# Performance work log

Measured on AMD Instinct MI355X. Metric: run time of the kernel, lower is better.

Reference implementation:

```python
import jax, jax.numpy as jnp
import numpy as np

B, N, C, H, P, DP = 2, 1024, 768, 12, 4, 64
CH = C // H
SCALE = CH ** -0.5
EPS = 1e-5


def setup_inputs() -> dict:
    key = jax.random.key(0)
    ks = jax.random.split(key, 24)
    w = lambda k, s: jax.random.normal(k, s, jnp.float32) * 0.02
    inp = {
        'single': jax.random.normal(ks[0], (B, N, C), jnp.float32),
        'pair': jax.random.normal(ks[1], (B, N, N, DP), jnp.float32),
        'rot': jax.random.normal(ks[2], (B, N, 3, 3), jnp.float32),
        'trans': jax.random.normal(ks[3], (B, N, 3), jnp.float32),
        'mask': jnp.ones((B, N), dtype=bool),
        'Wq': w(ks[4], (C, C)), 'bq': jnp.zeros((C,), jnp.float32),
        'Wk': w(ks[5], (C, C)), 'bk': jnp.zeros((C,), jnp.float32),
        'Wv': w(ks[6], (C, C)), 'bv': jnp.zeros((C,), jnp.float32),
        'Wpb': w(ks[7], (DP, H)), 'bpb': jnp.zeros((H,), jnp.float32),
        'Wqp': w(ks[8], (C, H * P * 3)), 'bqp': jnp.zeros((H * P * 3,), jnp.float32),
        'Wkp': w(ks[9], (C, H * P * 3)), 'bkp': jnp.zeros((H * P * 3,), jnp.float32),
        'Wvp': w(ks[10], (C, H * P * 3)), 'bvp': jnp.zeros((H * P * 3,), jnp.float32),
        'Wo': w(ks[11], (C, C)), 'bo': jnp.zeros((C,), jnp.float32),
        'Wpo': w(ks[12], (H * P * 3, C)), 'bpo': jnp.zeros((C,), jnp.float32),
        'gamma': jnp.ones((C,), jnp.float32), 'beta': jnp.zeros((C,), jnp.float32),
    }
    return inp


def _ipa(single, pair, rot, trans, mask,
         Wq, bq, Wk, bk, Wv, bv, Wpb, bpb,
         Wqp, bqp, Wkp, bkp, Wvp, bvp,
         Wo, bo, Wpo, bpo, gamma, beta):
    # scalar q/k/v: [B,N,H,CH]
    q = (single @ Wq + bq).reshape(B, N, H, CH)
    k = (single @ Wk + bk).reshape(B, N, H, CH)
    v = (single @ Wv + bv).reshape(B, N, H, CH)
    # pair bias: [B,H,N,N]
    pair_bias = jnp.transpose(pair @ Wpb + bpb, (0, 3, 1, 2))
    # point q/k/v in local frames: [B,N,H,P,3]
    q_pts = (single @ Wqp + bqp).reshape(B, N, H, P, 3)
    k_pts = (single @ Wkp + bkp).reshape(B, N, H, P, 3)
    v_pts = (single @ Wvp + bvp).reshape(B, N, H, P, 3)
    # rotate into global frame and translate
    t = trans[:, :, None, None, :]  # [B,N,1,1,3]
    rt = lambda pts: jnp.einsum('bnhpd,bnde->bnhpe', pts, rot) + t
    q_pts, k_pts, v_pts = rt(q_pts), rt(k_pts), rt(v_pts)
    # squared norms: [B,H,N]
    q2 = jnp.transpose((q_pts ** 2).sum((3, 4)), (0, 2, 1))
    k2 = jnp.transpose((k_pts ** 2).sum((3, 4)), (0, 2, 1))
    # logits [B,H,M,N]
    scalar_logits = jnp.einsum('bmhc,bnhc->bhmn', q, k) * SCALE
    qk_pts = jnp.einsum('bmhpd,bnhpd->bhmn', q_pts, k_pts)
    point_logits = -0.5 * (q2[:, :, :, None] + k2[:, :, None, :] - 2.0 * qk_pts) * SCALE
    logits = scalar_logits + point_logits + pair_bias
    mask2d = mask[:, None, :, None] & mask[:, None, None, :]
    logits = jnp.where(mask2d, logits, -1e9)
    attn = jax.nn.softmax(logits, axis=-1)
    # dual output aggregation
    out_scalar = jnp.einsum('bhmn,bnhc->bmhc', attn, v).reshape(B, N, C)
    out_points = jnp.einsum('bhmn,bnhpd->bmhpd', attn, v_pts).reshape(B, N, H * P * 3)
    out = (out_scalar @ Wo + bo) + (out_points @ Wpo + bpo)
    x = single + out
    mu = x.mean(-1, keepdims=True)
    var = ((x - mu) ** 2).mean(-1, keepdims=True)
    return (x - mu) * jax.lax.rsqrt(var + EPS) * gamma + beta


def reference(single, pair, rot, trans, mask,
              Wq, bq, Wk, bk, Wv, bv, Wpb, bpb,
              Wqp, bqp, Wkp, bkp, Wvp, bvp,
              Wo, bo, Wpo, bpo, gamma, beta):
    return _ipa(single, pair, rot, trans, mask,
                Wq, bq, Wk, bk, Wv, bv, Wpb, bpb,
                Wqp, bqp, Wkp, bkp, Wvp, bvp,
                Wo, bo, Wpo, bpo, gamma, beta)
```

## Files before the change

kernel.cpp:

```cpp
#include <hip/hip_runtime.h>
#include <hip/hip_bf16.h>

#define B_ 2
#define N_ 1024
#define C_ 768
#define H_ 12
#define CH_ 64
#define P_ 4
#define DP_ 64
#define HP3 144
#define SCALE_ 0.125f
#define FATS 2816
#define K2_ 960

typedef __attribute__((ext_vector_type(8))) short short8;
typedef __attribute__((ext_vector_type(4))) float f32x4;

__device__ __forceinline__ short f2bf(float f) {
  __hip_bfloat16 h = __float2bfloat16(f);
  return *reinterpret_cast<short*>(&h);
}
__device__ __forceinline__ float bf2f(unsigned short u) {
  __hip_bfloat16 h;
  *reinterpret_cast<unsigned short*>(&h) = u;
  return __bfloat162float(h);
}

__global__ __launch_bounds__(256) void convert_single(
    const float* __restrict__ src, unsigned short* __restrict__ dst)
{
  const int idx = blockIdx.x * 256 + threadIdx.x;
  const float4 v = reinterpret_cast<const float4*>(src)[idx];
  union { unsigned short u[4]; uint2 v2; } o;
  o.u[0] = (unsigned short)f2bf(v.x); o.u[1] = (unsigned short)f2bf(v.y);
  o.u[2] = (unsigned short)f2bf(v.z); o.u[3] = (unsigned short)f2bf(v.w);
  reinterpret_cast<uint2*>(dst)[idx] = o.v2;
}

__global__ __launch_bounds__(256) void pack_w1(
    const float* __restrict__ Wq, const float* __restrict__ Wk,
    const float* __restrict__ Wv, const float* __restrict__ Wqp,
    const float* __restrict__ Wkp, const float* __restrict__ Wvp,
    unsigned short* __restrict__ WT)
{
  __shared__ float t[16][17];
  const int tid = threadIdx.x;
  const int rr = tid >> 4, cc = tid & 15;
  const int kk0 = blockIdx.x * 16;
  const int nn0 = blockIdx.y * 16;
  const float* W = nullptr; int ncol0 = 0, Nw = 768;
  if (nn0 < 2304) {
    int s = nn0 / 768;
    W = (s == 0) ? Wq : (s == 1 ? Wk : Wv);
    ncol0 = nn0 - s * 768; Nw = 768;
  } else if (nn0 < 2736) {
    int s = (nn0 - 2304) / 144;
    W = (s == 0) ? Wqp : (s == 1 ? Wkp : Wvp);
    ncol0 = nn0 - 2304 - s * 144; Nw = 144;
  }
  t[rr][cc] = W ? W[(size_t)(kk0 + rr) * Nw + ncol0 + cc] : 0.f;
  __syncthreads();
  WT[(size_t)(nn0 + rr) * 768 + kk0 + cc] = (unsigned short)f2bf(t[cc][rr]);
}

__global__ __launch_bounds__(256) void pack_w2(
    const float* __restrict__ Wo, const float* __restrict__ Wpo,
    unsigned short* __restrict__ WT)
{
  __shared__ float t[16][17];
  const int tid = threadIdx.x;
  const int rr = tid >> 4, cc = tid & 15;
  const int kk0 = blockIdx.x * 16;
  const int nn0 = blockIdx.y * 16;
  const int k2 = kk0 + rr, h = k2 / 80, c80 = k2 - h * 80;
  float v = 0.f;
  if (c80 < 64)      v = Wo[(size_t)(h * 64 + c80) * 768 + nn0 + cc];
  else if (c80 < 76) v = Wpo[(size_t)(h * 12 + c80 - 64) * 768 + nn0 + cc];
  t[rr][cc] = v;
  __syncthreads();
  WT[(size_t)(nn0 + rr) * 960 + kk0 + cc] = (unsigned short)f2bf(t[cc][rr]);
}

__global__ __launch_bounds__(256) void pack_bias(
    const float* __restrict__ bq, const float* __restrict__ bk,
    const float* __restrict__ bv, const float* __restrict__ bqp,
    const float* __restrict__ bkp, const float* __restrict__ bvp,
    const float* __restrict__ bo, const float* __restrict__ bpo,
    float* __restrict__ bcat1, float* __restrict__ bias2)
{
  const int idx = blockIdx.x * 256 + threadIdx.x;
  if (idx < 2816) {
    float v = 0.f;
    if (idx < 2304) { int s = idx / 768; const float* p = s == 0 ? bq : (s == 1 ? bk : bv); v = p[idx - s * 768]; }
    else if (idx < 2736) { int s = (idx - 2304) / 144; const float* p = s == 0 ? bqp : (s == 1 ? bkp : bvp); v = p[idx - 2304 - s * 144]; }
    bcat1[idx] = v;
  }
  if (idx < 768) bias2[idx] = bo[idx] + bpo[idx];
}

__global__ __launch_bounds__(256) void gemm_bf16(
    const unsigned short* __restrict__ A, int lda,
    const unsigned short* __restrict__ BT, int ldb, int K,
    float* __restrict__ out, int ldo, const float* __restrict__ bias)
{
  __shared__ __align__(16) unsigned short As[128][40];
  __shared__ __align__(16) unsigned short Bs[128][40];
  const int tid = threadIdx.x;
  const int w = tid >> 6, l = tid & 63, r16 = l & 15, g = l >> 4;
  const int wr = w >> 1, wc = w & 1;
  const int bm = blockIdx.y * 128, bn = blockIdx.x * 128;
  f32x4 acc[4][4];
  #pragma unroll
  for (int mi = 0; mi < 4; ++mi)
    #pragma unroll
    for (int nj = 0; nj < 4; ++nj) {
      acc[mi][nj][0] = 0.f; acc[mi][nj][1] = 0.f;
      acc[mi][nj][2] = 0.f; acc[mi][nj][3] = 0.f;
    }
  for (int k0 = 0; k0 < K; k0 += 32) {
    #pragma unroll
    for (int i = 0; i < 2; ++i) {
      const int idx = tid + 256 * i;
      const int row = idx >> 2, q4 = idx & 3;
      *(uint4*)&As[row][q4 * 8] =
          *(const uint4*)&A[(size_t)(bm + row) * lda + k0 + q4 * 8];
      *(uint4*)&Bs[row][q4 * 8] =
          *(const uint4*)&BT[(size_t)(bn + row) * ldb + k0 + q4 * 8];
    }
    __syncthreads();
    short8 af[4], bfr[4];
    #pragma unroll
    for (int mi = 0; mi < 4; ++mi)
      af[mi] = *(const short8*)&As[wr * 64 + mi * 16 + r16][g * 8];
    #pragma unroll
    for (int nj = 0; nj < 4; ++nj)
      bfr[nj] = *(const short8*)&Bs[wc * 64 + nj * 16 + r16][g * 8];
    #pragma unroll
    for (int mi = 0; mi < 4; ++mi)
      #pragma unroll
      for (int nj = 0; nj < 4; ++nj)
        acc[mi][nj] = __builtin_amdgcn_mfma_f32_16x16x32_bf16(
            af[mi], bfr[nj], acc[mi][nj], 0, 0, 0);
    __syncthreads();
  }
  #pragma unroll
  for (int mi = 0; mi < 4; ++mi)
    #pragma unroll
    for (int nj = 0; nj < 4; ++nj) {
      const int n = bn + wc * 64 + nj * 16 + r16;
      const float bn_ = bias[n];
      #pragma unroll
      for (int reg = 0; reg < 4; ++reg) {
        const int m = bm + wr * 64 + mi * 16 + g * 4 + reg;
        out[(size_t)m * ldo + n] = acc[mi][nj][reg] + bn_;
      }
    }
}

__global__ __launch_bounds__(256) void pts_transform(
    float* __restrict__ fat, int col0, const float* __restrict__ rot,
    const float* __restrict__ trans, float* __restrict__ sq)
{
  int idx = blockIdx.x * 256 + threadIdx.x;
  if (idx >= B_ * N_ * H_) return;
  int h  = idx % H_;
  int bn = idx / H_;
  int b = bn >> 10, n = bn & 1023;
  float r[9], t[3];
  #pragma unroll
  for (int i = 0; i < 9; i++) r[i] = rot[(size_t)bn * 9 + i];
  #pragma unroll
  for (int i = 0; i < 3; i++) t[i] = trans[(size_t)bn * 3 + i];
  float* base = fat + (size_t)bn * FATS + col0 + h * 12;
  float s = 0.f;
  #pragma unroll
  for (int p = 0; p < P_; p++) {
    float d0 = base[p * 3 + 0], d1 = base[p * 3 + 1], d2 = base[p * 3 + 2];
    #pragma unroll
    for (int e = 0; e < 3; e++) {
      float o = d0 * r[0 * 3 + e] + d1 * r[1 * 3 + e] + d2 * r[2 * 3 + e] + t[e];
      base[p * 3 + e] = o;
      s += o * o;
    }
  }
  if (sq) sq[((size_t)b * H_ + h) * N_ + n] = s;
}

__global__ __launch_bounds__(128) void augment_kernel(
    const float* __restrict__ fat,
    const float* __restrict__ q2b, const float* __restrict__ k2b,
    __hip_bfloat16* __restrict__ Qaug, __hip_bfloat16* __restrict__ Kaug,
    __hip_bfloat16* __restrict__ Vtg)
{
  const int c = threadIdx.x;
  const int bn = blockIdx.x, h = blockIdx.y;
  const int b = bn >> 10, n = bn & 1023;
  const int bh = b * H_ + h;
  const float* row = fat + (size_t)bn * FATS;
  if (c < 96) {
    float qv, kv;
    if (c < 64) {
      qv = SCALE_ * row[h * CH_ + c];
      kv = row[768 + h * CH_ + c];
    } else if (c < 76) {
      qv = SCALE_ * row[2304 + h * 12 + (c - 64)];
      kv = row[2448 + h * 12 + (c - 64)];
    } else if (c == 76) {
      qv = -0.5f * SCALE_ * q2b[((size_t)bh << 10) + n];
      kv = 1.0f;
    } else if (c == 77) {
      qv = -0.5f * SCALE_;
      kv = k2b[((size_t)bh << 10) + n];
    } else { qv = 0.f; kv = 0.f; }
    const size_t orow = ((size_t)bh << 10) + n;
    Qaug[orow * 96 + c] = __float2bfloat16(qv);
    Kaug[orow * 96 + c] = __float2bfloat16(kv);
  }
  if (c < 80) {
    float vv = 0.f;
    if (c < 64) vv = row[1536 + h * CH_ + c];
    else if (c < 76) vv = row[2592 + h * 12 + (c - 64)];
    Vtg[(((size_t)bh * 80 + c) << 10) + n] = __float2bfloat16(vv);
  }
}

__global__ __launch_bounds__(256) void pair_bias_mfma(
    const float* __restrict__ pair, const float* __restrict__ Wpb,
    const float* __restrict__ bpb, unsigned short* __restrict__ pb)
{
  __shared__ __align__(16) short WpbT[16][72];
  __shared__ float bpb_s[16];
  __shared__ unsigned short PBs[256][18];
  const int tid = threadIdx.x;
  const int w = tid >> 6, l = tid & 63, r16 = l & 15, g = l >> 4;
  const size_t F0 = (size_t)blockIdx.x * 256;
  const int b = (int)(F0 >> 20);
  const int mn0 = (int)(F0 & 1048575);
  #pragma unroll
  for (int i = 0; i < 4; ++i) {
    int idx = tid + 256 * i;
    int hh = idx & 15, d = idx >> 4;
    WpbT[hh][d] = f2bf(hh < 12 ? Wpb[d * 12 + hh] : 0.f);
  }
  if (tid < 16) bpb_s[tid] = (tid < 12) ? bpb[tid] : 0.f;
  __syncthreads();
  const float4* p4 = (const float4*)pair;
  #pragma unroll
  for (int rg = 0; rg < 4; ++rg) {
    const size_t Fr = F0 + w * 64 + rg * 16 + r16;
    const float bias = bpb_s[r16];
    f32x4 acc;
    acc[0] = bias; acc[1] = bias; acc[2] = bias; acc[3] = bias;
    #pragma unroll
    for (int ks = 0; ks < 2; ++ks) {
      const float4 a0 = p4[Fr * 16 + g * 2 + ks * 8];
      const float4 a1 = p4[Fr * 16 + g * 2 + ks * 8 + 1];
      short8 ap;
      ap[0] = f2bf(a0.x); ap[1] = f2bf(a0.y); ap[2] = f2bf(a0.z); ap[3] = f2bf(a0.w);
      ap[4] = f2bf(a1.x); ap[5] = f2bf(a1.y); ap[6] = f2bf(a1.z); ap[7] = f2bf(a1.w);
      const short8 bw = *(const short8*)&WpbT[r16][ks * 32 + g * 8];
      acc = __builtin_amdgcn_mfma_f32_16x16x32_bf16(ap, bw, acc, 0, 0, 0);
    }
    #pragma unroll
    for (int reg = 0; reg < 4; ++reg)
      PBs[w * 64 + rg * 16 + 4 * g + reg][r16] = (unsigned short)f2bf(acc[reg]);
  }
  __syncthreads();
  #pragma unroll
  for (int hh = 0; hh < 12; ++hh)
    pb[((size_t)(b * 12 + hh) << 20) + mn0 + tid] = PBs[tid][hh];
}

__global__ __launch_bounds__(256) void flash_attn(
    const __hip_bfloat16* __restrict__ Qaug, const __hip_bfloat16* __restrict__ Kaug,
    const __hip_bfloat16* __restrict__ Vtg, const unsigned short* __restrict__ pb,
    unsigned short* __restrict__ fused)
{
  __shared__ __align__(16) short Qs[64][104];
  __shared__ __align__(16) short Ks[64][104];
  __shared__ __align__(16) short Vt[80][72];
  __shared__ __align__(16) short Ps[64][72];
  const int tid = threadIdx.x;
  const int w = tid >> 6, l = tid & 63, r16 = l & 15, g = l >> 4;
  const int m0 = blockIdx.x * 64;
  const int h = blockIdx.y, b = blockIdx.z;
  const int bh = b * H_ + h;
  const uint4* Qg = (const uint4*)Qaug;
  const uint4* Kg = (const uint4*)Kaug;
  const uint4* Vg = (const uint4*)Vtg;
  {
    const int r = tid >> 2, q = tid & 3;
    #pragma unroll
    for (int i = 0; i < 3; ++i) {
      const int c8 = q + 4 * i;
      *(uint4*)&Qs[r][c8 * 8] = Qg[(size_t)((bh << 10) + m0 + r) * 12 + c8];
    }
  }
  float rm[4], rl[4];
  f32x4 acc[5];
  #pragma unroll
  for (int r = 0; r < 4; ++r) { rm[r] = -1e30f; rl[r] = 0.f; }
  #pragma unroll
  for (int ct = 0; ct < 5; ++ct) {
    acc[ct][0] = 0.f; acc[ct][1] = 0.f; acc[ct][2] = 0.f; acc[ct][3] = 0.f;
  }
  __syncthreads();
  for (int t = 0; t < 16; ++t) {
    const int n0 = t * 64;
    {
      const int r = tid >> 2, q = tid & 3;
      #pragma unroll
      for (int i = 0; i < 3; ++i) {
        const int c8 = q + 4 * i;
        *(uint4*)&Ks[r][c8 * 8] = Kg[(size_t)((bh << 10) + n0 + r) * 12 + c8];
      }
      #pragma unroll
      for (int i = 0; i < 3; ++i) {
        const int ch = tid + 256 * i;
        if (ch < 640) {
          const int c = ch >> 3, j8 = ch & 7;
          *(uint4*)&Vt[c][j8 * 8] = Vg[(size_t)(bh * 80 + c) * 128 + (n0 >> 3) + j8];
        }
      }
    }
    f32x4 s[4];
    {
      const unsigned short* pbrow = pb + ((size_t)bh << 20) + n0 + r16;
      #pragma unroll
      for (int j = 0; j < 4; ++j)
        #pragma unroll
        for (int reg = 0; reg < 4; ++reg)
          s[j][reg] = bf2f(pbrow[((size_t)(m0 + w * 16 + 4 * g + reg) << 10) + 16 * j]);
    }
    __syncthreads();
    #pragma unroll
    for (int ks = 0; ks < 3; ++ks) {
      const short8 aQ = *(const short8*)&Qs[w * 16 + r16][ks * 32 + g * 8];
      #pragma unroll
      for (int j = 0; j < 4; ++j) {
        const short8 bK = *(const short8*)&Ks[16 * j + r16][ks * 32 + g * 8];
        s[j] = __builtin_amdgcn_mfma_f32_16x16x32_bf16(aQ, bK, s[j], 0, 0, 0);
      }
    }
    #pragma unroll
    for (int reg = 0; reg < 4; ++reg) {
      float tm = fmaxf(fmaxf(s[0][reg], s[1][reg]), fmaxf(s[2][reg], s[3][reg]));
      tm = fmaxf(tm, __shfl_xor(tm, 1));
      tm = fmaxf(tm, __shfl_xor(tm, 2));
      tm = fmaxf(tm, __shfl_xor(tm, 4));
      tm = fmaxf(tm, __shfl_xor(tm, 8));
      const float nm = fmaxf(rm[reg], tm);
      const float fac = __expf(rm[reg] - nm);
      rm[reg] = nm;
      float ps = 0.f;
      #pragma unroll
      for (int j = 0; j < 4; ++j) {
        const float p = __expf(s[j][reg] - nm);
        s[j][reg] = p;
        ps += p;
      }
      ps += __shfl_xor(ps, 1);
      ps += __shfl_xor(ps, 2);
      ps += __shfl_xor(ps, 4);
      ps += __shfl_xor(ps, 8);
      rl[reg] = rl[reg] * fac + ps;
      #pragma unroll
      for (int ct = 0; ct < 5; ++ct) acc[ct][reg] *= fac;
    }
    #pragma unroll
    for (int j = 0; j < 4; ++j)
      #pragma unroll
      for (int reg = 0; reg < 4; ++reg)
        Ps[w * 16 + 4 * g + reg][16 * j + r16] = f2bf(s[j][reg]);
    __syncthreads();
    #pragma unroll
    for (int ks = 0; ks < 2; ++ks) {
      const short8 aP = *(const short8*)&Ps[w * 16 + r16][ks * 32 + g * 8];
      #pragma unroll
      for (int ct = 0; ct < 5; ++ct) {
        const short8 bV = *(const short8*)&Vt[ct * 16 + r16][ks * 32 + g * 8];
        acc[ct] = __builtin_amdgcn_mfma_f32_16x16x32_bf16(aP, bV, acc[ct], 0, 0, 0);
      }
    }
    __syncthreads();
  }
  #pragma unroll
  for (int reg = 0; reg < 4; ++reg) {
    const float inv = 1.f / rl[reg];
    const size_t mg = (size_t)(b * N_ + m0 + w * 16 + 4 * g + reg);
    #pragma unroll
    for (int ct = 0; ct < 5; ++ct)
      fused[mg * K2_ + h * 80 + ct * 16 + r16] =
          (unsigned short)f2bf(acc[ct][reg] * inv);
  }
}

__global__ __launch_bounds__(256) void ln_kernel(
    const float* __restrict__ single, const float* __restrict__ tmp,
    const float* __restrict__ gamma, const float* __restrict__ beta,
    float* __restrict__ out)
{
  __shared__ float x_s[C_];
  __shared__ float rs1[4], rs2[4];
  const int row = blockIdx.x, tid = threadIdx.x;
  const int lane = tid & 63, wave = tid >> 6;
  const size_t base = (size_t)row * C_;
  float s1 = 0.f, s2 = 0.f;
  for (int i = tid; i < C_; i += 256) {
    float x = single[base + i] + tmp[base + i];
    x_s[i] = x;
    s1 += x;
    s2 += x * x;
  }
  #pragma unroll
  for (int off = 32; off > 0; off >>= 1) {
    s1 += __shfl_xor(s1, off);
    s2 += __shfl_xor(s2, off);
  }
  if (!lane) { rs1[wave] = s1; rs2[wave] = s2; }
  __syncthreads();
  const float S1 = rs1[0] + rs1[1] + rs1[2] + rs1[3];
  const float S2 = rs2[0] + rs2[1] + rs2[2] + rs2[3];
  const float mu = S1 * (1.f / C_);
  const float var = S2 * (1.f / C_) - mu * mu;
  const float inv = rsqrtf(var + 1e-5f);
  for (int i = tid; i < C_; i += 256)
    out[base + i] = (x_s[i] - mu) * inv * gamma[i] + beta[i];
}

extern "C" void kernel_launch(void* const* d_in, const int* in_sizes, int n_in,
                              void* d_out, int out_size, void* d_ws, size_t ws_size,
                              hipStream_t stream) {
  const float* single = (const float*)d_in[0];
  const float* pair   = (const float*)d_in[1];
  const float* rot    = (const float*)d_in[2];
  const float* trans  = (const float*)d_in[3];
  const float* Wq  = (const float*)d_in[5];
  const float* bq  = (const float*)d_in[6];
  const float* Wk  = (const float*)d_in[7];
  const float* bk  = (const float*)d_in[8];
  const float* Wv  = (const float*)d_in[9];
  const float* bv  = (const float*)d_in[10];
  const float* Wpb = (const float*)d_in[11];
  const float* bpb = (const float*)d_in[12];
  const float* Wqp = (const float*)d_in[13];
  const float* bqp = (const float*)d_in[14];
  const float* Wkp = (const float*)d_in[15];
  const float* bkp = (const float*)d_in[16];
  const float* Wvp = (const float*)d_in[17];
  const float* bvp = (const float*)d_in[18];
  const float* Wo  = (const float*)d_in[19];
  const float* bo  = (const float*)d_in[20];
  const float* Wpo = (const float*)d_in[21];
  const float* bpo = (const float*)d_in[22];
  const float* gamma = (const float*)d_in[23];
  const float* beta  = (const float*)d_in[24];

  float* ws = (float*)d_ws;
  float* fat  = ws;
  float* q2b  = ws + 5767168;
  float* k2b  = ws + 5791744;
  float* tmpb = ws + 5816320;
  unsigned short* pbb  = (unsigned short*)(ws + 7389184);
  __hip_bfloat16* Qaug = (__hip_bfloat16*)(ws + 19972096);
  __hip_bfloat16* Kaug = (__hip_bfloat16*)(ws + 21151744);
  __hip_bfloat16* Vtg  = (__hip_bfloat16*)(ws + 22331392);
  unsigned short* Sbf  = (unsigned short*)(ws + 23314432);
  unsigned short* WT1  = (unsigned short*)(ws + 24100864);
  unsigned short* W2T  = (unsigned short*)(ws + 25182208);
  float* bcat1 = ws + 25550848;
  float* bias2 = ws + 25553664;
  unsigned short* fusedb = (unsigned short*)(ws + 25554432);

  const dim3 blk(256);
  convert_single<<<1536, blk, 0, stream>>>(single, Sbf);
  pack_w1<<<dim3(48, 176), blk, 0, stream>>>(Wq, Wk, Wv, Wqp, Wkp, Wvp, WT1);
  pack_w2<<<dim3(60, 48), blk, 0, stream>>>(Wo, Wpo, W2T);
  pack_bias<<<11, blk, 0, stream>>>(bq, bk, bv, bqp, bkp, bvp, bo, bpo, bcat1, bias2);
  gemm_bf16<<<dim3(22, 16), blk, 0, stream>>>(Sbf, 768, WT1, 768, 768, fat, FATS, bcat1);
  pts_transform<<<96, blk, 0, stream>>>(fat, 2304, rot, trans, q2b);
  pts_transform<<<96, blk, 0, stream>>>(fat, 2448, rot, trans, k2b);
  pts_transform<<<96, blk, 0, stream>>>(fat, 2592, rot, trans, nullptr);
  augment_kernel<<<dim3(2048, 12), dim3(128), 0, stream>>>(fat, q2b, k2b, Qaug, Kaug, Vtg);
  pair_bias_mfma<<<8192, blk, 0, stream>>>(pair, Wpb, bpb, pbb);
  flash_attn<<<dim3(16, 12, 2), blk, 0, stream>>>(Qaug, Kaug, Vtg, pbb, fusedb);
  gemm_bf16<<<dim3(6, 16), blk, 0, stream>>>(fusedb, K2_, W2T, K2_, K2_, tmpb, 768, bias2);
  ln_kernel<<<2048, blk, 0, stream>>>(single, tmpb, gamma, beta, (float*)d_out);
}
```

Measured before the change: 284.4 us.

## Split flash attention over key chunks, fuse prep kernels, shrink GEMM tiles

```diff
diff --git a/kernel.cpp b/kernel.cpp
--- a/kernel.cpp
+++ b/kernel.cpp
@@ -12,6 +12,7 @@
 #define SCALE_ 0.125f
 #define FATS 2816
 #define K2_ 960
+#define NCHUNK 2
 
 typedef __attribute__((ext_vector_type(8))) short short8;
 typedef __attribute__((ext_vector_type(4))) float f32x4;
@@ -26,191 +27,183 @@
   return __bfloat162float(h);
 }
 
-__global__ __launch_bounds__(256) void convert_single(
-    const float* __restrict__ src, unsigned short* __restrict__ dst)
-{
-  const int idx = blockIdx.x * 256 + threadIdx.x;
-  const float4 v = reinterpret_cast<const float4*>(src)[idx];
-  union { unsigned short u[4]; uint2 v2; } o;
-  o.u[0] = (unsigned short)f2bf(v.x); o.u[1] = (unsigned short)f2bf(v.y);
-  o.u[2] = (unsigned short)f2bf(v.z); o.u[3] = (unsigned short)f2bf(v.w);
-  reinterpret_cast<uint2*>(dst)[idx] = o.v2;
-}
-
-__global__ __launch_bounds__(256) void pack_w1(
+__global__ __launch_bounds__(256) void prep_misc(
+    const float* __restrict__ single, unsigned short* __restrict__ Sbf,
     const float* __restrict__ Wq, const float* __restrict__ Wk,
     const float* __restrict__ Wv, const float* __restrict__ Wqp,
     const float* __restrict__ Wkp, const float* __restrict__ Wvp,
-    unsigned short* __restrict__ WT)
-{
-  __shared__ float t[16][17];
-  const int tid = threadIdx.x;
-  const int rr = tid >> 4, cc = tid & 15;
-  const int kk0 = blockIdx.x * 16;
-  const int nn0 = blockIdx.y * 16;
-  const float* W = nullptr; int ncol0 = 0, Nw = 768;
-  if (nn0 < 2304) {
-    int s = nn0 / 768;
-    W = (s == 0) ? Wq : (s == 1 ? Wk : Wv);
-    ncol0 = nn0 - s * 768; Nw = 768;
-  } else if (nn0 < 2736) {
-    int s = (nn0 - 2304) / 144;
-    W = (s == 0) ? Wqp : (s == 1 ? Wkp : Wvp);
-    ncol0 = nn0 - 2304 - s * 144; Nw = 144;
-  }
-  t[rr][cc] = W ? W[(size_t)(kk0 + rr) * Nw + ncol0 + cc] : 0.f;
-  __syncthreads();
-  WT[(size_t)(nn0 + rr) * 768 + kk0 + cc] = (unsigned short)f2bf(t[cc][rr]);
-}
-
-__global__ __launch_bounds__(256) void pack_w2(
+    unsigned short* __restrict__ WT1,
     const float* __restrict__ Wo, const float* __restrict__ Wpo,
-    unsigned short* __restrict__ WT)
-{
-  __shared__ float t[16][17];
-  const int tid = threadIdx.x;
-  const int rr = tid >> 4, cc = tid & 15;
-  const int kk0 = blockIdx.x * 16;
-  const int nn0 = blockIdx.y * 16;
-  const int k2 = kk0 + rr, h = k2 / 80, c80 = k2 - h * 80;
-  float v = 0.f;
-  if (c80 < 64)      v = Wo[(size_t)(h * 64 + c80) * 768 + nn0 + cc];
-  else if (c80 < 76) v = Wpo[(size_t)(h * 12 + c80 - 64) * 768 + nn0 + cc];
-  t[rr][cc] = v;
-  __syncthreads();
-  WT[(size_t)(nn0 + rr) * 960 + kk0 + cc] = (unsigned short)f2bf(t[cc][rr]);
-}
-
-__global__ __launch_bounds__(256) void pack_bias(
+    unsigned short* __restrict__ W2T,
     const float* __restrict__ bq, const float* __restrict__ bk,
     const float* __restrict__ bv, const float* __restrict__ bqp,
     const float* __restrict__ bkp, const float* __restrict__ bvp,
     const float* __restrict__ bo, const float* __restrict__ bpo,
     float* __restrict__ bcat1, float* __restrict__ bias2)
 {
-  const int idx = blockIdx.x * 256 + threadIdx.x;
-  if (idx < 2816) {
+  __shared__ float t[16][17];
+  const int tid = threadIdx.x;
+  const int bid = blockIdx.x;
+  if (bid < 8448) {
+    const int bx = bid % 48, by = bid / 48;
+    const int rr = tid >> 4, cc = tid & 15;
+    const int kk0 = bx * 16, nn0 = by * 16;
+    const float* W = nullptr; int ncol0 = 0, Nw = 768;
+    if (nn0 < 2304) {
+      int s = nn0 / 768;
+      W = (s == 0) ? Wq : (s == 1 ? Wk : Wv);
+      ncol0 = nn0 - s * 768; Nw = 768;
+    } else if (nn0 < 2736) {
+      int s = (nn0 - 2304) / 144;
+      W = (s == 0) ? Wqp : (s == 1 ? Wkp : Wvp);
+      ncol0 = nn0 - 2304 - s * 144; Nw = 144;
+    }
+    t[rr][cc] = W ? W[(size_t)(kk0 + rr) * Nw + ncol0 + cc] : 0.f;
+    __syncthreads();
+    WT1[(size_t)(nn0 + rr) * 768 + kk0 + cc] = (unsigned short)f2bf(t[cc][rr]);
+  } else if (bid < 11328) {
+    const int lb = bid - 8448;
+    const int bx = lb % 60, by = lb / 60;
+    const int rr = tid >> 4, cc = tid & 15;
+    const int kk0 = bx * 16, nn0 = by * 16;
+    const int k2 = kk0 + rr, h = k2 / 80, c80 = k2 - h * 80;
     float v = 0.f;
-    if (idx < 2304) { int s = idx / 768; const float* p = s == 0 ? bq : (s == 1 ? bk : bv); v = p[idx - s * 768]; }
-    else if (idx < 2736) { int s = (idx - 2304) / 144; const float* p = s == 0 ? bqp : (s == 1 ? bkp : bvp); v = p[idx - 2304 - s * 144]; }
-    bcat1[idx] = v;
-  }
-  if (idx < 768) bias2[idx] = bo[idx] + bpo[idx];
-}
-
+    if (c80 < 64)      v = Wo[(size_t)(h * 64 + c80) * 768 + nn0 + cc];
+    else if (c80 < 76) v = Wpo[(size_t)(h * 12 + c80 - 64) * 768 + nn0 + cc];
+    t[rr][cc] = v;
+    __syncthreads();
+    W2T[(size_t)(nn0 + rr) * 960 + kk0 + cc] = (unsigned short)f2bf(t[cc][rr]);
+  } else if (bid < 11339) {
+    const int idx = (bid - 11328) * 256 + tid;
+    if (idx < 2816) {
+      float v = 0.f;
+      if (idx < 2304) { int s = idx / 768; const float* p = s == 0 ? bq : (s == 1 ? bk : bv); v = p[idx - s * 768]; }
+      else if (idx < 2736) { int s = (idx - 2304) / 144; const float* p = s == 0 ? bqp : (s == 1 ? bkp : bvp); v = p[idx - 2304 - s * 144]; }
+      bcat1[idx] = v;
+    }
+    if (idx < 768) bias2[idx] = bo[idx] + bpo[idx];
+  } else {
+    const int idx = (bid - 11339) * 256 + tid;
+    const float4 v = reinterpret_cast<const float4*>(single)[idx];
+    union { unsigned short u[4]; uint2 v2; } o;
+    o.u[0] = (unsigned short)f2bf(v.x); o.u[1] = (unsigned short)f2bf(v.y);
+    o.u[2] = (unsigned short)f2bf(v.z); o.u[3] = (unsigned short)f2bf(v.w);
+    reinterpret_cast<uint2*>(Sbf)[idx] = o.v2;
+  }
+}
+
+template<int BM>
 __global__ __launch_bounds__(256) void gemm_bf16(
     const unsigned short* __restrict__ A, int lda,
     const unsigned short* __restrict__ BT, int ldb, int K,
     float* __restrict__ out, int ldo, const float* __restrict__ bias)
 {
-  __shared__ __align__(16) unsigned short As[128][40];
-  __shared__ __align__(16) unsigned short Bs[128][40];
+  constexpr int BN = 64;
+  constexpr int MI = BM / 32;
+  constexpr int NJ = 2;
+  __shared__ __align__(16) unsigned short As[BM][40];
+  __shared__ __align__(16) unsigned short Bs[BN][40];
   const int tid = threadIdx.x;
   const int w = tid >> 6, l = tid & 63, r16 = l & 15, g = l >> 4;
   const int wr = w >> 1, wc = w & 1;
-  const int bm = blockIdx.y * 128, bn = blockIdx.x * 128;
-  f32x4 acc[4][4];
-  #pragma unroll
-  for (int mi = 0; mi < 4; ++mi)
-    #pragma unroll
-    for (int nj = 0; nj < 4; ++nj) {
+  const int bm = blockIdx.y * BM, bn = blockIdx.x * BN;
+  f32x4 acc[MI][NJ];
+  #pragma unroll
+  for (int mi = 0; mi < MI; ++mi)
+    #pragma unroll
+    for (int nj = 0; nj < NJ; ++nj) {
       acc[mi][nj][0] = 0.f; acc[mi][nj][1] = 0.f;
       acc[mi][nj][2] = 0.f; acc[mi][nj][3] = 0.f;
     }
   for (int k0 = 0; k0 < K; k0 += 32) {
     #pragma unroll
-    for (int i = 0; i < 2; ++i) {
+    for (int i = 0; i < BM / 64; ++i) {
       const int idx = tid + 256 * i;
       const int row = idx >> 2, q4 = idx & 3;
       *(uint4*)&As[row][q4 * 8] =
           *(const uint4*)&A[(size_t)(bm + row) * lda + k0 + q4 * 8];
-      *(uint4*)&Bs[row][q4 * 8] =
-          *(const uint4*)&BT[(size_t)(bn + row) * ldb + k0 + q4 * 8];
-    }
-    __syncthreads();
-    short8 af[4], bfr[4];
-    #pragma unroll
-    for (int mi = 0; mi < 4; ++mi)
-      af[mi] = *(const short8*)&As[wr * 64 + mi * 16 + r16][g * 8];
-    #pragma unroll
-    for (int nj = 0; nj < 4; ++nj)
-      bfr[nj] = *(const short8*)&Bs[wc * 64 + nj * 16 + r16][g * 8];
-    #pragma unroll
-    for (int mi = 0; mi < 4; ++mi)
-      #pragma unroll
-      for (int nj = 0; nj < 4; ++nj)
+    }
+    {
+      const int row = tid >> 2, q4 = tid & 3;
+      if (row < BN)
+        *(uint4*)&Bs[row][q4 * 8] =
+            *(const uint4*)&BT[(size_t)(bn + row) * ldb + k0 + q4 * 8];
+    }
+    __syncthreads();
+    short8 af[MI], bfr[NJ];
+    #pragma unroll
+    for (int mi = 0; mi < MI; ++mi)
+      af[mi] = *(const short8*)&As[wr * (BM / 2) + mi * 16 + r16][g * 8];
+    #pragma unroll
+    for (int nj = 0; nj < NJ; ++nj)
+      bfr[nj] = *(const short8*)&Bs[wc * 32 + nj * 16 + r16][g * 8];
+    #pragma unroll
+    for (int mi = 0; mi < MI; ++mi)
+      #pragma unroll
+      for (int nj = 0; nj < NJ; ++nj)
         acc[mi][nj] = __builtin_amdgcn_mfma_f32_16x16x32_bf16(
             af[mi], bfr[nj], acc[mi][nj], 0, 0, 0);
     __syncthreads();
   }
   #pragma unroll
-  for (int mi = 0; mi < 4; ++mi)
-    #pragma unroll
-    for (int nj = 0; nj < 4; ++nj) {
-      const int n = bn + wc * 64 + nj * 16 + r16;
+  for (int mi = 0; mi < MI; ++mi)
+    #pragma unroll
+    for (int nj = 0; nj < NJ; ++nj) {
+      const int n = bn + wc * 32 + nj * 16 + r16;
       const float bn_ = bias[n];
       #pragma unroll
       for (int reg = 0; reg < 4; ++reg) {
-        const int m = bm + wr * 64 + mi * 16 + g * 4 + reg;
+        const int m = bm + wr * (BM / 2) + mi * 16 + g * 4 + reg;
         out[(size_t)m * ldo + n] = acc[mi][nj][reg] + bn_;
       }
     }
 }
 
-__global__ __launch_bounds__(256) void pts_transform(
-    float* __restrict__ fat, int col0, const float* __restrict__ rot,
-    const float* __restrict__ trans, float* __restrict__ sq)
-{
-  int idx = blockIdx.x * 256 + threadIdx.x;
-  if (idx >= B_ * N_ * H_) return;
-  int h  = idx % H_;
-  int bn = idx / H_;
-  int b = bn >> 10, n = bn & 1023;
-  float r[9], t[3];
-  #pragma unroll
-  for (int i = 0; i < 9; i++) r[i] = rot[(size_t)bn * 9 + i];
-  #pragma unroll
-  for (int i = 0; i < 3; i++) t[i] = trans[(size_t)bn * 3 + i];
-  float* base = fat + (size_t)bn * FATS + col0 + h * 12;
-  float s = 0.f;
-  #pragma unroll
-  for (int p = 0; p < P_; p++) {
-    float d0 = base[p * 3 + 0], d1 = base[p * 3 + 1], d2 = base[p * 3 + 2];
-    #pragma unroll
-    for (int e = 0; e < 3; e++) {
-      float o = d0 * r[0 * 3 + e] + d1 * r[1 * 3 + e] + d2 * r[2 * 3 + e] + t[e];
-      base[p * 3 + e] = o;
-      s += o * o;
-    }
-  }
-  if (sq) sq[((size_t)b * H_ + h) * N_ + n] = s;
-}
-
-__global__ __launch_bounds__(128) void augment_kernel(
-    const float* __restrict__ fat,
-    const float* __restrict__ q2b, const float* __restrict__ k2b,
+__global__ __launch_bounds__(128) void prep_qkv(
+    const float* __restrict__ fat, const float* __restrict__ rot,
+    const float* __restrict__ trans,
     __hip_bfloat16* __restrict__ Qaug, __hip_bfloat16* __restrict__ Kaug,
     __hip_bfloat16* __restrict__ Vtg)
 {
-  const int c = threadIdx.x;
+  __shared__ float pts[3][12];
+  __shared__ float s2[2];
+  const int tid = threadIdx.x;
   const int bn = blockIdx.x, h = blockIdx.y;
   const int b = bn >> 10, n = bn & 1023;
   const int bh = b * H_ + h;
   const float* row = fat + (size_t)bn * FATS;
+  if (tid < 36) {
+    const int set = tid / 12, j = tid - set * 12;
+    const int p = j / 3, e = j - p * 3;
+    const float* src = row + 2304 + set * 144 + h * 12 + p * 3;
+    const float d0 = src[0], d1 = src[1], d2 = src[2];
+    const float* rr = rot + (size_t)bn * 9;
+    pts[set][j] = d0 * rr[e] + d1 * rr[3 + e] + d2 * rr[6 + e]
+                  + trans[(size_t)bn * 3 + e];
+  }
+  __syncthreads();
+  if (tid < 2) {
+    float s = 0.f;
+    #pragma unroll
+    for (int j = 0; j < 12; ++j) s += pts[tid][j] * pts[tid][j];
+    s2[tid] = s;
+  }
+  __syncthreads();
+  const int c = tid;
   if (c < 96) {
     float qv, kv;
     if (c < 64) {
       qv = SCALE_ * row[h * CH_ + c];
       kv = row[768 + h * CH_ + c];
     } else if (c < 76) {
-      qv = SCALE_ * row[2304 + h * 12 + (c - 64)];
-      kv = row[2448 + h * 12 + (c - 64)];
+      qv = SCALE_ * pts[0][c - 64];
+      kv = pts[1][c - 64];
     } else if (c == 76) {
-      qv = -0.5f * SCALE_ * q2b[((size_t)bh << 10) + n];
+      qv = -0.5f * SCALE_ * s2[0];
       kv = 1.0f;
     } else if (c == 77) {
       qv = -0.5f * SCALE_;
-      kv = k2b[((size_t)bh << 10) + n];
+      kv = s2[1];
     } else { qv = 0.f; kv = 0.f; }
     const size_t orow = ((size_t)bh << 10) + n;
     Qaug[orow * 96 + c] = __float2bfloat16(qv);
@@ -219,7 +212,7 @@
   if (c < 80) {
     float vv = 0.f;
     if (c < 64) vv = row[1536 + h * CH_ + c];
-    else if (c < 76) vv = row[2592 + h * 12 + (c - 64)];
+    else if (c < 76) vv = pts[2][c - 64];
     Vtg[(((size_t)bh * 80 + c) << 10) + n] = __float2bfloat16(vv);
   }
 }
@@ -271,30 +264,29 @@
     pb[((size_t)(b * 12 + hh) << 20) + mn0 + tid] = PBs[tid][hh];
 }
 
-__global__ __launch_bounds__(256) void flash_attn(
+__global__ __launch_bounds__(256) void flash_attn_part(
     const __hip_bfloat16* __restrict__ Qaug, const __hip_bfloat16* __restrict__ Kaug,
     const __hip_bfloat16* __restrict__ Vtg, const unsigned short* __restrict__ pb,
-    unsigned short* __restrict__ fused)
-{
-  __shared__ __align__(16) short Qs[64][104];
+    float* __restrict__ pacc, float* __restrict__ pml)
+{
   __shared__ __align__(16) short Ks[64][104];
   __shared__ __align__(16) short Vt[80][72];
   __shared__ __align__(16) short Ps[64][72];
   const int tid = threadIdx.x;
   const int w = tid >> 6, l = tid & 63, r16 = l & 15, g = l >> 4;
   const int m0 = blockIdx.x * 64;
-  const int h = blockIdx.y, b = blockIdx.z;
+  const int h = blockIdx.y;
+  const int b = blockIdx.z >> 1, chunk = blockIdx.z & 1;
   const int bh = b * H_ + h;
-  const uint4* Qg = (const uint4*)Qaug;
   const uint4* Kg = (const uint4*)Kaug;
   const uint4* Vg = (const uint4*)Vtg;
+  short8 qreg[3];
   {
-    const int r = tid >> 2, q = tid & 3;
-    #pragma unroll
-    for (int i = 0; i < 3; ++i) {
-      const int c8 = q + 4 * i;
-      *(uint4*)&Qs[r][c8 * 8] = Qg[(size_t)((bh << 10) + m0 + r) * 12 + c8];
-    }
+    const unsigned short* qrow =
+        (const unsigned short*)Qaug + (size_t)((bh << 10) + m0 + w * 16 + r16) * 96;
+    #pragma unroll
+    for (int ks = 0; ks < 3; ++ks)
+      qreg[ks] = *(const short8*)&qrow[ks * 32 + g * 8];
   }
   float rm[4], rl[4];
   f32x4 acc[5];
@@ -304,8 +296,7 @@
   for (int ct = 0; ct < 5; ++ct) {
     acc[ct][0] = 0.f; acc[ct][1] = 0.f; acc[ct][2] = 0.f; acc[ct][3] = 0.f;
   }
-  __syncthreads();
-  for (int t = 0; t < 16; ++t) {
+  for (int t = chunk * (16 / NCHUNK); t < (chunk + 1) * (16 / NCHUNK); ++t) {
     const int n0 = t * 64;
     {
       const int r = tid >> 2, q = tid & 3;
@@ -318,8 +309,8 @@
       for (int i = 0; i < 3; ++i) {
         const int ch = tid + 256 * i;
         if (ch < 640) {
-          const int c = ch >> 3, j8 = ch & 7;
-          *(uint4*)&Vt[c][j8 * 8] = Vg[(size_t)(bh * 80 + c) * 128 + (n0 >> 3) + j8];
+          const int cc = ch >> 3, j8 = ch & 7;
+          *(uint4*)&Vt[cc][j8 * 8] = Vg[(size_t)(bh * 80 + cc) * 128 + (n0 >> 3) + j8];
         }
       }
     }
@@ -335,11 +326,10 @@
     __syncthreads();
     #pragma unroll
     for (int ks = 0; ks < 3; ++ks) {
-      const short8 aQ = *(const short8*)&Qs[w * 16 + r16][ks * 32 + g * 8];
       #pragma unroll
       for (int j = 0; j < 4; ++j) {
         const short8 bK = *(const short8*)&Ks[16 * j + r16][ks * 32 + g * 8];
-        s[j] = __builtin_amdgcn_mfma_f32_16x16x32_bf16(aQ, bK, s[j], 0, 0, 0);
+        s[j] = __builtin_amdgcn_mfma_f32_16x16x32_bf16(qreg[ks], bK, s[j], 0, 0, 0);
       }
     }
     #pragma unroll
@@ -386,12 +376,39 @@
   }
   #pragma unroll
   for (int reg = 0; reg < 4; ++reg) {
-    const float inv = 1.f / rl[reg];
-    const size_t mg = (size_t)(b * N_ + m0 + w * 16 + 4 * g + reg);
+    const int row = (bh << 10) + m0 + w * 16 + 4 * g + reg;
+    const size_t base = ((size_t)chunk * 24576 + row) * 80;
     #pragma unroll
     for (int ct = 0; ct < 5; ++ct)
-      fused[mg * K2_ + h * 80 + ct * 16 + r16] =
-          (unsigned short)f2bf(acc[ct][reg] * inv);
+      pacc[base + ct * 16 + r16] = acc[ct][reg];
+    if (r16 == 0) {
+      pml[((size_t)chunk * 24576 + row) * 2]     = rm[reg];
+      pml[((size_t)chunk * 24576 + row) * 2 + 1] = rl[reg];
+    }
+  }
+}
+
+__global__ __launch_bounds__(256) void flash_combine(
+    const float* __restrict__ pacc, const float* __restrict__ pml,
+    unsigned short* __restrict__ fused)
+{
+  const int tid = threadIdx.x;
+  const int r = tid >> 4, cg = tid & 15;
+  const int row = blockIdx.x * 16 + r;
+  const int bh = row >> 10, m = row & 1023;
+  const int b = bh / 12, h = bh - b * 12;
+  const float m0 = pml[(size_t)row * 2], l0 = pml[(size_t)row * 2 + 1];
+  const float m1 = pml[((size_t)24576 + row) * 2], l1 = pml[((size_t)24576 + row) * 2 + 1];
+  const float M = fmaxf(m0, m1);
+  const float w0 = __expf(m0 - M), w1 = __expf(m1 - M);
+  const float inv = 1.f / (l0 * w0 + l1 * w1);
+  const size_t mg = (size_t)(b * N_ + m);
+  #pragma unroll
+  for (int i = 0; i < 5; ++i) {
+    const int c = cg * 5 + i;
+    const float a0 = pacc[(size_t)row * 80 + c];
+    const float a1 = pacc[((size_t)24576 + row) * 80 + c];
+    fused[mg * K2_ + h * 80 + c] = (unsigned short)f2bf((a0 * w0 + a1 * w1) * inv);
   }
 }
 
@@ -458,32 +475,32 @@
 
   float* ws = (float*)d_ws;
   float* fat  = ws;
-  float* q2b  = ws + 5767168;
-  float* k2b  = ws + 5791744;
-  float* tmpb = ws + 5816320;
-  unsigned short* pbb  = (unsigned short*)(ws + 7389184);
-  __hip_bfloat16* Qaug = (__hip_bfloat16*)(ws + 19972096);
-  __hip_bfloat16* Kaug = (__hip_bfloat16*)(ws + 21151744);
-  __hip_bfloat16* Vtg  = (__hip_bfloat16*)(ws + 22331392);
-  unsigned short* Sbf  = (unsigned short*)(ws + 23314432);
-  unsigned short* WT1  = (unsigned short*)(ws + 24100864);
-  unsigned short* W2T  = (unsigned short*)(ws + 25182208);
-  float* bcat1 = ws + 25550848;
-  float* bias2 = ws + 25553664;
-  unsigned short* fusedb = (unsigned short*)(ws + 25554432);
+  float* tmpb = ws + 5767168;
+  unsigned short* pbb  = (unsigned short*)(ws + 7340032);
+  __hip_bfloat16* Qaug = (__hip_bfloat16*)(ws + 19922944);
+  __hip_bfloat16* Kaug = (__hip_bfloat16*)(ws + 21102592);
+  __hip_bfloat16* Vtg  = (__hip_bfloat16*)(ws + 22282240);
+  unsigned short* Sbf  = (unsigned short*)(ws + 23265280);
+  unsigned short* WT1  = (unsigned short*)(ws + 24051712);
+  unsigned short* W2T  = (unsigned short*)(ws + 25133056);
+  float* bcat1 = ws + 25501696;
+  float* bias2 = ws + 25504512;
+  unsigned short* fusedb = (unsigned short*)(ws + 25505536);
+  float* pacc = ws + 26488576;
+  float* pml  = ws + 30420736;
 
   const dim3 blk(256);
-  convert_single<<<1536, blk, 0, stream>>>(single, Sbf);
-  pack_w1<<<dim3(48, 176), blk, 0, stream>>>(Wq, Wk, Wv, Wqp, Wkp, Wvp, WT1);
-  pack_w2<<<dim3(60, 48), blk, 0, stream>>>(Wo, Wpo, W2T);
-  pack_bias<<<11, blk, 0, stream>>>(bq, bk, bv, bqp, bkp, bvp, bo, bpo, bcat1, bias2);
-  gemm_bf16<<<dim3(22, 16), blk, 0, stream>>>(Sbf, 768, WT1, 768, 768, fat, FATS, bcat1);
-  pts_transform<<<96, blk, 0, stream>>>(fat, 2304, rot, trans, q2b);
-  pts_transform<<<96, blk, 0, stream>>>(fat, 2448, rot, trans, k2b);
-  pts_transform<<<96, blk, 0, stream>>>(fat, 2592, rot, trans, nullptr);
-  augment_kernel<<<dim3(2048, 12), dim3(128), 0, stream>>>(fat, q2b, k2b, Qaug, Kaug, Vtg);
+  prep_misc<<<12875, blk, 0, stream>>>(single, Sbf, Wq, Wk, Wv, Wqp, Wkp, Wvp,
+                                       WT1, Wo, Wpo, W2T, bq, bk, bv, bqp, bkp,
+                                       bvp, bo, bpo, bcat1, bias2);
+  gemm_bf16<128><<<dim3(44, 16), blk, 0, stream>>>(Sbf, 768, WT1, 768, 768,
+                                                   fat, FATS, bcat1);
+  prep_qkv<<<dim3(2048, 12), dim3(128), 0, stream>>>(fat, rot, trans, Qaug, Kaug, Vtg);
   pair_bias_mfma<<<8192, blk, 0, stream>>>(pair, Wpb, bpb, pbb);
-  flash_attn<<<dim3(16, 12, 2), blk, 0, stream>>>(Qaug, Kaug, Vtg, pbb, fusedb);
-  gemm_bf16<<<dim3(6, 16), blk, 0, stream>>>(fusedb, K2_, W2T, K2_, K2_, tmpb, 768, bias2);
+  flash_attn_part<<<dim3(16, 12, 2 * NCHUNK), blk, 0, stream>>>(
+      Qaug, Kaug, Vtg, pbb, pacc, pml);
+  flash_combine<<<1536, blk, 0, stream>>>(pacc, pml, fusedb);
+  gemm_bf16<64><<<dim3(12, 32), blk, 0, stream>>>(fusedb, K2_, W2T, K2_, K2_,
+                                                  tmpb, 768, bias2);
   ln_kernel<<<2048, blk, 0, stream>>>(single, tmpb, gamma, beta, (float*)d_out);
 }
```

New measurement: 249.3 us. -12.3%, faster.
